# Optimization experiments

Measured on AMD Instinct MI355X. Metric: run time of the kernel, lower is better.

## Reference

```python
import jax, jax.numpy as jnp
import numpy as np

NEG_INF = -1e25


def setup_inputs() -> dict:
    key = jax.random.key(0)
    ks = jax.random.split(key, 7)
    B, L, Q, H = 4, 512, 64, 768
    bert = jax.random.normal(ks[0], (B, L, H), dtype=jnp.float32)
    query = jax.random.normal(ks[1], (B, Q, H), dtype=jnp.float32)
    mask = jax.random.randint(ks[2], (B, L), 0, 2).astype(bool)
    # nn.Linear(2H, H): weight (H, 2H), bias (H)
    W_w = jax.random.normal(ks[3], (H, 2 * H), dtype=jnp.float32) * (1.0 / np.sqrt(2 * H))
    W_b = jax.random.normal(ks[4], (H,), dtype=jnp.float32) * 0.02
    # nn.Linear(H, 1): weight (1, H), bias (1)
    v_w = jax.random.normal(ks[5], (1, H), dtype=jnp.float32) * (1.0 / np.sqrt(H))
    v_b = jax.random.normal(ks[6], (1,), dtype=jnp.float32) * 0.02
    return {"bert": bert, "query": query, "mask": mask,
            "W_w": W_w, "W_b": W_b, "v_w": v_w, "v_b": v_b}


def reference(bert, query, mask, W_w, W_b, v_w, v_b):
    H = bert.shape[-1]
    # Linear(cat([bert, query])) = bert @ Wb^T + query @ Wq^T + b  (avoids the (B,Q,L,2H) concat)
    W_bert = W_w[:, :H]    # (H, H) acts on bert part
    W_query = W_w[:, H:]   # (H, H) acts on query part
    bp = jnp.einsum('blh,kh->blk', bert, W_bert)     # (B, L, H)
    qp = jnp.einsum('bqh,kh->bqk', query, W_query)   # (B, Q, H)
    h = jnp.tanh(bp[:, None, :, :] + qp[:, :, None, :] + W_b)  # (B, Q, L, H)
    x = jnp.einsum('bqlh,h->bql', h, v_w[0]) + v_b[0]           # (B, Q, L)
    x = jnp.where(mask[:, None, :], x, NEG_INF)
    return jax.nn.softmax(x, axis=-1)
```

## Files before the change

kernel.cpp:

```cpp
#include <hip/hip_runtime.h>
#include <hip/hip_bf16.h>

#define LOG2E    1.4426950408889634f
#define TWOLOG2E 2.8853900817779268f

typedef short bf16x8 __attribute__((ext_vector_type(8)));
typedef float f32x4  __attribute__((ext_vector_type(4)));

static __device__ __forceinline__ float bf16_to_f(unsigned short u) {
    union { unsigned int i; float f; } v; v.i = ((unsigned int)u) << 16; return v.f;
}
static __device__ __forceinline__ unsigned short f_to_bf16_rne(float x) {
    union { float f; unsigned int i; } v; v.f = x;
    unsigned int lsb = (v.i >> 16) & 1u;
    v.i += 0x7fffu + lsb;
    return (unsigned short)(v.i >> 16);
}

__device__ __forceinline__ float tanh_fast(float x) {
    float e = __builtin_amdgcn_exp2f(x * TWOLOG2E);
    return 1.0f - 2.0f * __builtin_amdgcn_rcpf(1.0f + e);
}

__global__ __launch_bounds__(256) void cast_split_all(
    const float* __restrict__ bert, const float* __restrict__ query,
    const float* __restrict__ Ww,
    unsigned short* __restrict__ Ahi, unsigned short* __restrict__ Alo,
    unsigned short* __restrict__ Whi, unsigned short* __restrict__ Wlo)
{
    const int i = blockIdx.x * 256 + threadIdx.x;
    float4 x;
    unsigned short* dh;
    unsigned short* dl;
    int di;
    if (i < 442368) {
        x  = (i < 393216) ? ((const float4*)bert)[i] : ((const float4*)query)[i - 393216];
        dh = Ahi; dl = Alo; di = i;
    } else {
        x  = ((const float4*)Ww)[i - 442368];
        dh = Whi; dl = Wlo; di = i - 442368;
    }
    ushort4 h, l;
    h.x = f_to_bf16_rne(x.x); l.x = f_to_bf16_rne(x.x - bf16_to_f(h.x));
    h.y = f_to_bf16_rne(x.y); l.y = f_to_bf16_rne(x.y - bf16_to_f(h.y));
    h.z = f_to_bf16_rne(x.z); l.z = f_to_bf16_rne(x.z - bf16_to_f(h.z));
    h.w = f_to_bf16_rne(x.w); l.w = f_to_bf16_rne(x.w - bf16_to_f(h.w));
    ((ushort4*)dh)[di] = h;
    ((ushort4*)dl)[di] = l;
}

__global__ __launch_bounds__(256) void gemm_mfma_split(
    const unsigned short* __restrict__ Ahi, const unsigned short* __restrict__ Alo,
    const unsigned short* __restrict__ Whi, const unsigned short* __restrict__ Wlo,
    const float* __restrict__ Wb, float* __restrict__ C)
{
    const int t  = threadIdx.x;
    const int wv = t >> 6;
    const int l  = t & 63;
    const int lr = l & 15;
    const int kg = l >> 4;
    const int n0 = blockIdx.x * 64;
    const int bm0 = blockIdx.y * 128;
    const int m0 = bm0 + wv * 32;
    const bool isq = (bm0 >= 2048);
    const int wsel = isq ? 1 : 0;

    const size_t aoff = (size_t)(m0 + lr) * 768 + kg * 8;
    const unsigned short* pAh = Ahi + aoff;
    const unsigned short* pAl = Alo + aoff;
    const size_t boff = (size_t)(2 * (n0 + lr) + wsel) * 768 + kg * 8;
    const unsigned short* pBh = Whi + boff;
    const unsigned short* pBl = Wlo + boff;

    f32x4 acc[2][4];
    #pragma unroll
    for (int i = 0; i < 2; ++i)
        #pragma unroll
        for (int j = 0; j < 4; ++j) acc[i][j] = (f32x4){0.f, 0.f, 0.f, 0.f};

    #pragma unroll 2
    for (int k0 = 0; k0 < 768; k0 += 32) {
        bf16x8 ah[2], al[2], bh[4], bl[4];
        #pragma unroll
        for (int i = 0; i < 2; ++i) {
            ah[i] = *(const bf16x8*)(pAh + (size_t)i * 16 * 768 + k0);
            al[i] = *(const bf16x8*)(pAl + (size_t)i * 16 * 768 + k0);
        }
        #pragma unroll
        for (int j = 0; j < 4; ++j) {
            bh[j] = *(const bf16x8*)(pBh + (size_t)j * 32 * 768 + k0);
            bl[j] = *(const bf16x8*)(pBl + (size_t)j * 32 * 768 + k0);
        }
        #pragma unroll
        for (int i = 0; i < 2; ++i)
            #pragma unroll
            for (int j = 0; j < 4; ++j) {
                acc[i][j] = __builtin_amdgcn_mfma_f32_16x16x32_bf16(ah[i], bh[j], acc[i][j], 0, 0, 0);
                acc[i][j] = __builtin_amdgcn_mfma_f32_16x16x32_bf16(ah[i], bl[j], acc[i][j], 0, 0, 0);
                acc[i][j] = __builtin_amdgcn_mfma_f32_16x16x32_bf16(al[i], bh[j], acc[i][j], 0, 0, 0);
            }
    }

    #pragma unroll
    for (int j = 0; j < 4; ++j) {
        const int col = n0 + j * 16 + lr;
        const float bias = isq ? Wb[col] : 0.f;
        #pragma unroll
        for (int i = 0; i < 2; ++i)
            #pragma unroll
            for (int r = 0; r < 4; ++r) {
                const int row = m0 + i * 16 + kg * 4 + r;
                C[(size_t)row * 768 + col] = acc[i][j][r] + bias;
            }
    }
}

__global__ __launch_bounds__(256) void attn_scores(
    const float* __restrict__ bp, const float* __restrict__ qpb,
    const float* __restrict__ v_w, const float* __restrict__ v_b,
    float* __restrict__ X)
{
    __shared__ __align__(16) float bpL[16][68];
    __shared__ __align__(16) float qpL[16][68];
    __shared__ __align__(16) float vwL[64];
    const int t   = threadIdx.x;
    const int b   = blockIdx.z;
    const int q0  = blockIdx.y * 16;
    const int l0  = blockIdx.x * 16;
    const int li  = t & 15;
    const int qi  = t >> 4;
    const int row = t >> 4;
    const int col = (t & 15) << 2;
    const float* bprow = bp  + (size_t)(b * 512 + l0 + row) * 768;
    const float* qprow = qpb + (size_t)(b * 64  + q0 + row) * 768;
    float acc = 0.f;

    for (int k0 = 0; k0 < 768; k0 += 64) {
        *(float4*)&bpL[row][col] = *(const float4*)(bprow + k0 + col);
        *(float4*)&qpL[row][col] = *(const float4*)(qprow + k0 + col);
        if (t < 16) *(float4*)&vwL[t << 2] = *(const float4*)(v_w + k0 + (t << 2));
        __syncthreads();
        #pragma unroll
        for (int kk = 0; kk < 64; kk += 4) {
            float4 b4 = *(const float4*)&bpL[li][kk];
            float4 q4 = *(const float4*)&qpL[qi][kk];
            float4 v4 = *(const float4*)&vwL[kk];
            acc = fmaf(tanh_fast(b4.x + q4.x), v4.x, acc);
            acc = fmaf(tanh_fast(b4.y + q4.y), v4.y, acc);
            acc = fmaf(tanh_fast(b4.z + q4.z), v4.z, acc);
            acc = fmaf(tanh_fast(b4.w + q4.w), v4.w, acc);
        }
        __syncthreads();
    }
    X[(size_t)(b * 64 + q0 + qi) * 512 + l0 + li] = acc + v_b[0];
}

__global__ __launch_bounds__(512) void softmax_mask(
    const float* __restrict__ X, const int* __restrict__ mask,
    float* __restrict__ out)
{
    const int bq  = blockIdx.x;
    const int b   = bq >> 6;
    const int l   = threadIdx.x;
    const int wid = l >> 6;
    __shared__ float red[8];

    float v = X[(size_t)bq * 512 + l];
    const bool mk = (mask[b * 512 + l] != 0);
    v = mk ? v : -1e25f;

    float m = v;
    #pragma unroll
    for (int o = 32; o; o >>= 1) m = fmaxf(m, __shfl_xor(m, o));
    if ((l & 63) == 0) red[wid] = m;
    __syncthreads();
    #pragma unroll
    for (int i = 0; i < 8; ++i) m = fmaxf(m, red[i]);

    float e = __builtin_amdgcn_exp2f((v - m) * LOG2E);
    float s = e;
    #pragma unroll
    for (int o = 32; o; o >>= 1) s += __shfl_xor(s, o);
    __syncthreads();
    if ((l & 63) == 0) red[wid] = s;
    __syncthreads();
    s = 0.f;
    #pragma unroll
    for (int i = 0; i < 8; ++i) s += red[i];

    out[(size_t)bq * 512 + l] = e / s;
}

extern "C" void kernel_launch(void* const* d_in, const int* in_sizes, int n_in,
                              void* d_out, int out_size, void* d_ws, size_t ws_size,
                              hipStream_t stream)
{
    const float* bert  = (const float*)d_in[0];
    const float* query = (const float*)d_in[1];
    const int*   mask  = (const int*)  d_in[2];
    const float* W_w   = (const float*)d_in[3];
    const float* W_b   = (const float*)d_in[4];
    const float* v_w   = (const float*)d_in[5];
    const float* v_b   = (const float*)d_in[6];

    float* C = (float*)d_ws;
    float* X = C + (size_t)2304 * 768;
    unsigned short* Ahi = (unsigned short*)(X + (size_t)256 * 512);
    unsigned short* Alo = Ahi + (size_t)2304 * 768;
    unsigned short* Whi = Alo + (size_t)2304 * 768;
    unsigned short* Wlo = Whi + (size_t)1536 * 768;
    float* out = (float*)d_out;

    cast_split_all<<<2880, 256, 0, stream>>>(bert, query, W_w, Ahi, Alo, Whi, Wlo);
    gemm_mfma_split<<<dim3(12, 18), 256, 0, stream>>>(Ahi, Alo, Whi, Wlo, W_b, C);
    attn_scores<<<dim3(32, 4, 4), 256, 0, stream>>>(C, C + (size_t)2048 * 768, v_w, v_b, X);
    softmax_mask<<<dim3(256), 512, 0, stream>>>(X, mask, out);
}
```

Before: 148.3 us.

## Pre-pack MFMA fragments, fold tanh scaling into weights, simplify score kernel

The cast kernel now writes the bf16 hi/lo splits directly in MFMA fragment order, so each GEMM wave reads contiguous 16-byte-per-lane chunks. The GEMM becomes one 64-thread wave per 32x32 tile, launched as many small blocks. The 2*log2(e) factor is folded into the weights and bias, and tanh is rewritten so the score kernel needs only exp2 and rcp per element, with the constant terms and v_b dropped because softmax ignores them. The score kernel drops its LDS staging and reads rows straight from global memory, relying on caches and risking less reuse.

```diff
diff --git a/kernel.cpp b/kernel.cpp
--- a/kernel.cpp
+++ b/kernel.cpp
@@ -6,6 +6,7 @@
 
 typedef short bf16x8 __attribute__((ext_vector_type(8)));
 typedef float f32x4  __attribute__((ext_vector_type(4)));
+typedef unsigned short u16x8 __attribute__((ext_vector_type(8)));
 
 static __device__ __forceinline__ float bf16_to_f(unsigned short u) {
     union { unsigned int i; float f; } v; v.i = ((unsigned int)u) << 16; return v.f;
@@ -17,84 +18,94 @@
     return (unsigned short)(v.i >> 16);
 }
 
-__device__ __forceinline__ float tanh_fast(float x) {
-    float e = __builtin_amdgcn_exp2f(x * TWOLOG2E);
-    return 1.0f - 2.0f * __builtin_amdgcn_rcpf(1.0f + e);
-}
-
-__global__ __launch_bounds__(256) void cast_split_all(
+__global__ __launch_bounds__(256) void cast_frag(
     const float* __restrict__ bert, const float* __restrict__ query,
     const float* __restrict__ Ww,
-    unsigned short* __restrict__ Ahi, unsigned short* __restrict__ Alo,
-    unsigned short* __restrict__ Whi, unsigned short* __restrict__ Wlo)
-{
-    const int i = blockIdx.x * 256 + threadIdx.x;
-    float4 x;
-    unsigned short* dh;
-    unsigned short* dl;
-    int di;
-    if (i < 442368) {
-        x  = (i < 393216) ? ((const float4*)bert)[i] : ((const float4*)query)[i - 393216];
-        dh = Ahi; dl = Alo; di = i;
+    unsigned short* __restrict__ Ahf, unsigned short* __restrict__ Alf,
+    unsigned short* __restrict__ Whf, unsigned short* __restrict__ Wlf)
+{
+    const int i    = blockIdx.x * 256 + threadIdx.x;
+    const int lane = i & 63;
+    const float* src;
+    float scale;
+    unsigned short *dh, *dl;
+    size_t di;
+    if (i < 221184) {
+        const int rest = i >> 6;
+        const int kt = rest % 24, mt = rest / 24;
+        const int m  = mt * 16 + (lane & 15);
+        src = ((m < 2048) ? bert + (size_t)m * 768
+                          : query + (size_t)(m - 2048) * 768)
+              + kt * 32 + (lane >> 4) * 8;
+        scale = 1.0f;
+        dh = Ahf; dl = Alf; di = (size_t)i * 8;
     } else {
-        x  = ((const float4*)Ww)[i - 442368];
-        dh = Whi; dl = Wlo; di = i - 442368;
-    }
-    ushort4 h, l;
-    h.x = f_to_bf16_rne(x.x); l.x = f_to_bf16_rne(x.x - bf16_to_f(h.x));
-    h.y = f_to_bf16_rne(x.y); l.y = f_to_bf16_rne(x.y - bf16_to_f(h.y));
-    h.z = f_to_bf16_rne(x.z); l.z = f_to_bf16_rne(x.z - bf16_to_f(h.z));
-    h.w = f_to_bf16_rne(x.w); l.w = f_to_bf16_rne(x.w - bf16_to_f(h.w));
-    ((ushort4*)dh)[di] = h;
-    ((ushort4*)dl)[di] = l;
-}
-
-__global__ __launch_bounds__(256) void gemm_mfma_split(
-    const unsigned short* __restrict__ Ahi, const unsigned short* __restrict__ Alo,
-    const unsigned short* __restrict__ Whi, const unsigned short* __restrict__ Wlo,
+        const int j = i - 221184;
+        const int rest = j >> 6;
+        const int kt = rest % 24, nt2 = rest / 24;
+        const int sel = nt2 >> 6 ? 1 : (nt2 >= 48);
+        const int n   = (nt2 - sel * 48) * 16 + (lane & 15);
+        src = Ww + (size_t)n * 1536 + sel * 768 + kt * 32 + (lane >> 4) * 8;
+        scale = TWOLOG2E;
+        dh = Whf; dl = Wlf; di = (size_t)j * 8;
+    }
+    float4 x0 = *(const float4*)src;
+    float4 x1 = *(const float4*)(src + 4);
+    float xs[8] = {x0.x * scale, x0.y * scale, x0.z * scale, x0.w * scale,
+                   x1.x * scale, x1.y * scale, x1.z * scale, x1.w * scale};
+    u16x8 h, l;
+    #pragma unroll
+    for (int e = 0; e < 8; ++e) {
+        unsigned short hh = f_to_bf16_rne(xs[e]);
+        h[e] = hh;
+        l[e] = f_to_bf16_rne(xs[e] - bf16_to_f(hh));
+    }
+    *(u16x8*)(dh + di) = h;
+    *(u16x8*)(dl + di) = l;
+}
+
+__global__ __launch_bounds__(64) void gemm_frag(
+    const unsigned short* __restrict__ Ahf, const unsigned short* __restrict__ Alf,
+    const unsigned short* __restrict__ Whf, const unsigned short* __restrict__ Wlf,
     const float* __restrict__ Wb, float* __restrict__ C)
 {
-    const int t  = threadIdx.x;
-    const int wv = t >> 6;
-    const int l  = t & 63;
-    const int lr = l & 15;
-    const int kg = l >> 4;
-    const int n0 = blockIdx.x * 64;
-    const int bm0 = blockIdx.y * 128;
-    const int m0 = bm0 + wv * 32;
-    const bool isq = (bm0 >= 2048);
-    const int wsel = isq ? 1 : 0;
-
-    const size_t aoff = (size_t)(m0 + lr) * 768 + kg * 8;
-    const unsigned short* pAh = Ahi + aoff;
-    const unsigned short* pAl = Alo + aoff;
-    const size_t boff = (size_t)(2 * (n0 + lr) + wsel) * 768 + kg * 8;
-    const unsigned short* pBh = Whi + boff;
-    const unsigned short* pBl = Wlo + boff;
-
-    f32x4 acc[2][4];
+    const int l    = threadIdx.x;
+    const int w    = blockIdx.x;
+    const int mt_w = w / 24;
+    const int nt_w = w % 24;
+    const int m0   = mt_w * 32;
+    const int n0   = nt_w * 32;
+    const bool isq = (m0 >= 2048);
+    const int  fmt = mt_w * 2;
+    const int  fnt = (isq ? 48 : 0) + nt_w * 2;
+    const int  lr  = l & 15;
+    const int  kg  = l >> 4;
+
+    const unsigned short* pAh = Ahf + (size_t)fmt * 12288 + l * 8;
+    const unsigned short* pAl = Alf + (size_t)fmt * 12288 + l * 8;
+    const unsigned short* pBh = Whf + (size_t)fnt * 12288 + l * 8;
+    const unsigned short* pBl = Wlf + (size_t)fnt * 12288 + l * 8;
+
+    f32x4 acc[2][2];
     #pragma unroll
     for (int i = 0; i < 2; ++i)
         #pragma unroll
-        for (int j = 0; j < 4; ++j) acc[i][j] = (f32x4){0.f, 0.f, 0.f, 0.f};
-
-    #pragma unroll 2
-    for (int k0 = 0; k0 < 768; k0 += 32) {
-        bf16x8 ah[2], al[2], bh[4], bl[4];
+        for (int j = 0; j < 2; ++j) acc[i][j] = (f32x4){0.f, 0.f, 0.f, 0.f};
+
+    #pragma unroll 4
+    for (int kt = 0; kt < 24; ++kt) {
+        bf16x8 ah[2], al[2], bh[2], bl[2];
         #pragma unroll
         for (int i = 0; i < 2; ++i) {
-            ah[i] = *(const bf16x8*)(pAh + (size_t)i * 16 * 768 + k0);
-            al[i] = *(const bf16x8*)(pAl + (size_t)i * 16 * 768 + k0);
-        }
-        #pragma unroll
-        for (int j = 0; j < 4; ++j) {
-            bh[j] = *(const bf16x8*)(pBh + (size_t)j * 32 * 768 + k0);
-            bl[j] = *(const bf16x8*)(pBl + (size_t)j * 32 * 768 + k0);
+            ah[i] = *(const bf16x8*)(pAh + (size_t)i * 12288 + kt * 512);
+            al[i] = *(const bf16x8*)(pAl + (size_t)i * 12288 + kt * 512);
+            bh[i] = *(const bf16x8*)(pBh + (size_t)i * 12288 + kt * 512);
+            bl[i] = *(const bf16x8*)(pBl + (size_t)i * 12288 + kt * 512);
         }
         #pragma unroll
         for (int i = 0; i < 2; ++i)
             #pragma unroll
-            for (int j = 0; j < 4; ++j) {
+            for (int j = 0; j < 2; ++j) {
                 acc[i][j] = __builtin_amdgcn_mfma_f32_16x16x32_bf16(ah[i], bh[j], acc[i][j], 0, 0, 0);
                 acc[i][j] = __builtin_amdgcn_mfma_f32_16x16x32_bf16(ah[i], bl[j], acc[i][j], 0, 0, 0);
                 acc[i][j] = __builtin_amdgcn_mfma_f32_16x16x32_bf16(al[i], bh[j], acc[i][j], 0, 0, 0);
@@ -102,9 +113,9 @@
     }
 
     #pragma unroll
-    for (int j = 0; j < 4; ++j) {
-        const int col = n0 + j * 16 + lr;
-        const float bias = isq ? Wb[col] : 0.f;
+    for (int j = 0; j < 2; ++j) {
+        const int col  = n0 + j * 16 + lr;
+        const float bias = isq ? Wb[col] * TWOLOG2E : 0.f;
         #pragma unroll
         for (int i = 0; i < 2; ++i)
             #pragma unroll
@@ -116,43 +127,27 @@
 }
 
 __global__ __launch_bounds__(256) void attn_scores(
-    const float* __restrict__ bp, const float* __restrict__ qpb,
-    const float* __restrict__ v_w, const float* __restrict__ v_b,
+    const float* __restrict__ C, const float* __restrict__ v_w,
     float* __restrict__ X)
 {
-    __shared__ __align__(16) float bpL[16][68];
-    __shared__ __align__(16) float qpL[16][68];
-    __shared__ __align__(16) float vwL[64];
-    const int t   = threadIdx.x;
-    const int b   = blockIdx.z;
-    const int q0  = blockIdx.y * 16;
-    const int l0  = blockIdx.x * 16;
-    const int li  = t & 15;
-    const int qi  = t >> 4;
-    const int row = t >> 4;
-    const int col = (t & 15) << 2;
-    const float* bprow = bp  + (size_t)(b * 512 + l0 + row) * 768;
-    const float* qprow = qpb + (size_t)(b * 64  + q0 + row) * 768;
+    const int t  = threadIdx.x;
+    const int b  = blockIdx.z;
+    const int q  = blockIdx.y * 16 + (t >> 4);
+    const int lx = blockIdx.x * 16 + (t & 15);
+    const float* pb = C + (size_t)(b * 512 + lx) * 768;
+    const float* pq = C + (size_t)(2048 + b * 64 + q) * 768;
     float acc = 0.f;
-
-    for (int k0 = 0; k0 < 768; k0 += 64) {
-        *(float4*)&bpL[row][col] = *(const float4*)(bprow + k0 + col);
-        *(float4*)&qpL[row][col] = *(const float4*)(qprow + k0 + col);
-        if (t < 16) *(float4*)&vwL[t << 2] = *(const float4*)(v_w + k0 + (t << 2));
-        __syncthreads();
-        #pragma unroll
-        for (int kk = 0; kk < 64; kk += 4) {
-            float4 b4 = *(const float4*)&bpL[li][kk];
-            float4 q4 = *(const float4*)&qpL[qi][kk];
-            float4 v4 = *(const float4*)&vwL[kk];
-            acc = fmaf(tanh_fast(b4.x + q4.x), v4.x, acc);
-            acc = fmaf(tanh_fast(b4.y + q4.y), v4.y, acc);
-            acc = fmaf(tanh_fast(b4.z + q4.z), v4.z, acc);
-            acc = fmaf(tanh_fast(b4.w + q4.w), v4.w, acc);
-        }
-        __syncthreads();
-    }
-    X[(size_t)(b * 64 + q0 + qi) * 512 + l0 + li] = acc + v_b[0];
+    #pragma unroll 4
+    for (int k = 0; k < 768; k += 4) {
+        float4 bv = *(const float4*)(pb + k);
+        float4 qv = *(const float4*)(pq + k);
+        float4 vv = *(const float4*)(v_w + k);
+        acc = fmaf(vv.x, __builtin_amdgcn_rcpf(1.0f + __builtin_amdgcn_exp2f(bv.x + qv.x)), acc);
+        acc = fmaf(vv.y, __builtin_amdgcn_rcpf(1.0f + __builtin_amdgcn_exp2f(bv.y + qv.y)), acc);
+        acc = fmaf(vv.z, __builtin_amdgcn_rcpf(1.0f + __builtin_amdgcn_exp2f(bv.z + qv.z)), acc);
+        acc = fmaf(vv.w, __builtin_amdgcn_rcpf(1.0f + __builtin_amdgcn_exp2f(bv.w + qv.w)), acc);
+    }
+    X[(size_t)(b * 64 + q) * 512 + lx] = -2.f * acc;
 }
 
 __global__ __launch_bounds__(512) void softmax_mask(
@@ -202,17 +197,18 @@
     const float* W_b   = (const float*)d_in[4];
     const float* v_w   = (const float*)d_in[5];
     const float* v_b   = (const float*)d_in[6];
+    (void)v_b;
 
     float* C = (float*)d_ws;
     float* X = C + (size_t)2304 * 768;
-    unsigned short* Ahi = (unsigned short*)(X + (size_t)256 * 512);
-    unsigned short* Alo = Ahi + (size_t)2304 * 768;
-    unsigned short* Whi = Alo + (size_t)2304 * 768;
-    unsigned short* Wlo = Whi + (size_t)1536 * 768;
+    unsigned short* Ahf = (unsigned short*)(X + (size_t)256 * 512);
+    unsigned short* Alf = Ahf + (size_t)2304 * 768;
+    unsigned short* Whf = Alf + (size_t)2304 * 768;
+    unsigned short* Wlf = Whf + (size_t)1536 * 768;
     float* out = (float*)d_out;
 
-    cast_split_all<<<2880, 256, 0, stream>>>(bert, query, W_w, Ahi, Alo, Whi, Wlo);
-    gemm_mfma_split<<<dim3(12, 18), 256, 0, stream>>>(Ahi, Alo, Whi, Wlo, W_b, C);
-    attn_scores<<<dim3(32, 4, 4), 256, 0, stream>>>(C, C + (size_t)2048 * 768, v_w, v_b, X);
+    cast_frag<<<1440, 256, 0, stream>>>(bert, query, W_w, Ahf, Alf, Whf, Wlf);
+    gemm_frag<<<1728, 64, 0, stream>>>(Ahf, Alf, Whf, Wlf, W_b, C);
+    attn_scores<<<dim3(32, 4, 4), 256, 0, stream>>>(C, v_w, X);
     softmax_mask<<<dim3(256), 512, 0, stream>>>(X, mask, out);
 }
```

Result: no change. 147.6 us (-0.5%).
